# Kernel optimization log

Hardware: AMD Instinct MI355X
Metric: run time of the kernel (lower is better)

Reference implementation:

```python
import jax, jax.numpy as jnp
import numpy as np

D = 512      # d_model
P = 128      # proj_len
H = 8        # nhead
MID = 24     # middle_dim (hardcoded in module)
HD = MID // H    # head_dim = 3
HDV = D // H     # head_dim_v = 64
SCALE = HD ** -0.5   # scaling == pscaling since head_dim == phead_dim


def setup_inputs() -> dict:
    key = jax.random.key(0)
    ks = jax.random.split(key, 12)
    L, B = 2048, 16
    def w(k, o, i):
        return jax.random.normal(k, (o, i), jnp.float32) * 0.02
    def b(o):
        return jnp.zeros((o,), jnp.float32)
    return {
        "x": jax.random.normal(ks[0], (L, B, D), jnp.float32),
        "px": jax.random.normal(ks[1], (P, B, D), jnp.float32),
        "mask": jax.random.randint(ks[2], (B, L), 0, 2).astype(bool),
        "Wpq": w(ks[3], MID, D), "bpq": b(MID),
        "Wq": w(ks[4], MID, D), "bq": b(MID),
        "Wql": w(ks[5], P * H, D), "bql": b(P * H),
        "Wpk": w(ks[6], MID, D), "bpk": b(MID),
        "Wpv": w(ks[7], D, D), "bpv": b(D),
        "Wk": w(ks[8], MID, D), "bk": b(MID),
        "Wv": w(ks[9], D, D), "bv": b(D),
        "Wo": w(ks[10], D, D), "bo": b(D),
        "gamma": jnp.ones((D,), jnp.float32),
        "beta": jnp.zeros((D,), jnp.float32),
    }


def _layernorm(x, g, b, eps=1e-5):
    m = x.mean(-1, keepdims=True)
    v = ((x - m) ** 2).mean(-1, keepdims=True)
    return (x - m) / jnp.sqrt(v + eps) * g + b


def reference(x, px, mask, Wpq, bpq, Wq, bq, Wql, bql, Wpk, bpk, Wpv, bpv,
              Wk, bk, Wv, bv, Wo, bo, gamma, beta):
    L, B, _ = x.shape
    BH = B * H
    # ---- stage 1: compress length L -> P via projected attention ----
    pk = (x @ Wpk.T + bpk).reshape(L, BH, HD)     # [L, BH, hd]
    pv = (x @ Wpv.T + bpv).reshape(L, BH, HDV)    # [L, BH, hdv]
    pq = (px @ Wpq.T + bpq).reshape(P, BH, HD) * SCALE
    pqk = jnp.einsum('pnh,lnh->npl', pq, pk)      # [BH, P, L]
    pqk = pqk.reshape(B, H, P, L)
    pqk = jnp.where(mask[:, None, None, :], -jnp.inf, pqk).reshape(BH, P, L)
    pqk = jax.nn.softmax(pqk, axis=-1)            # dropout1 omitted (eval)
    pc = jnp.einsum('npl,lnv->npv', pqk, pv)      # [BH, P, hdv]
    pc = pc.transpose(1, 0, 2).reshape(P, B, D)   # compressed context
    # ---- stage 2: attention within compressed length P ----
    q_len = (x @ Wql.T + bql).reshape(L, BH, P).transpose(1, 0, 2)  # [BH, L, P]
    k = (pc @ Wk.T + bk).reshape(P, BH, HD).transpose(1, 0, 2)      # [BH, P, hd]
    v = (pc @ Wv.T + bv).reshape(P, BH, HDV).transpose(1, 0, 2)     # [BH, P, hdv]
    q = ((pc @ Wq.T + bq) * SCALE).reshape(P, BH, HD).transpose(1, 0, 2)
    aw = jax.nn.softmax(q @ k.transpose(0, 2, 1), axis=-1)  # [BH, P, P], dropout2 omitted
    attn = aw @ v                                            # [BH, P, hdv]
    attn = attn.transpose(1, 0, 2).reshape(P, B, D)
    attn = _layernorm(attn, gamma, beta)
    attn = attn.reshape(P, BH, HDV).transpose(1, 0, 2)       # [BH, P, hdv]
    # ---- stage 3: re-expand P -> L via learned length softmax ----
    ql = jax.nn.softmax(q_len, axis=-1)                      # dropout3 omitted
    out = (ql @ attn).transpose(1, 0, 2).reshape(L, B, D)
    return (out @ Wo.T + bo, pc)
```

## Files before the change

### kernel.cpp

```cpp
#include <hip/hip_runtime.h>
#include <cstdint>

#define L_    2048
#define B_    16
#define D_    512
#define P_    128
#define H_    8
#define MID_  24
#define HD_   3
#define HDV_  64
#define BH_   128
#define SCALE_ 0.57735026918962576f
#define S1C   4
#define S1L   (L_ / S1C)

typedef short  short8  __attribute__((ext_vector_type(8)));
typedef short  short4v __attribute__((ext_vector_type(4)));
typedef float  f32x4   __attribute__((ext_vector_type(4)));

__device__ __forceinline__ short f2bf(float f) {
    unsigned u = __builtin_bit_cast(unsigned, f);
    unsigned r = (u + 0x7fffu + ((u >> 16) & 1u)) >> 16;
    return (short)(unsigned short)r;
}

__device__ __forceinline__ int swz_off(int row, int chunk) {
    return row * 32 + ((chunk ^ ((row >> 1) & 3)) << 3);
}

__device__ __forceinline__ float block_reduce_sum_256(float v, volatile float* scratch) {
#pragma unroll
    for (int o = 32; o > 0; o >>= 1) v += __shfl_down(v, o, 64);
    int wid = threadIdx.x >> 6;
    if ((threadIdx.x & 63) == 0) scratch[wid] = v;
    __syncthreads();
    if (threadIdx.x == 0) scratch[4] = scratch[0] + scratch[1] + scratch[2] + scratch[3];
    __syncthreads();
    return scratch[4];
}

__global__ __launch_bounds__(256) void cvt_bf16(
    const float* __restrict__ src, short* __restrict__ dst, int n4)
{
    int i = blockIdx.x * 256 + threadIdx.x;
    if (i < n4) {
        float4 v = reinterpret_cast<const float4*>(src)[i];
        short4v o;
        o[0] = f2bf(v.x); o[1] = f2bf(v.y); o[2] = f2bf(v.z); o[3] = f2bf(v.w);
        reinterpret_cast<short4v*>(dst)[i] = o;
    }
}

__global__ __launch_bounds__(256) void gemm_bias(
    const float* __restrict__ A, const float* __restrict__ W,
    const float* __restrict__ bias, float* __restrict__ C,
    int M, int N, int K, float scale)
{
    __shared__ float As[32][36];
    __shared__ float Ws[64][36];
    const int t    = threadIdx.x;
    const int row0 = blockIdx.y * 32;
    const int col0 = blockIdx.x * 64;
    const int ty = t >> 4;
    const int tx = t & 15;
    const int lr  = t >> 3;
    const int lc4 = (t & 7) * 4;

    float acc[2][4] = {{0.f,0.f,0.f,0.f},{0.f,0.f,0.f,0.f}};

    for (int kk0 = 0; kk0 < K; kk0 += 32) {
        {
            float4 a = *reinterpret_cast<const float4*>(&A[(size_t)(row0 + lr) * K + kk0 + lc4]);
            *reinterpret_cast<float4*>(&As[lr][lc4]) = a;
        }
#pragma unroll
        for (int i = 0; i < 2; ++i) {
            int wr   = i * 32 + lr;
            int wcol = col0 + wr;
            float4 w = make_float4(0.f, 0.f, 0.f, 0.f);
            if (wcol < N)
                w = *reinterpret_cast<const float4*>(&W[(size_t)wcol * K + kk0 + lc4]);
            *reinterpret_cast<float4*>(&Ws[wr][lc4]) = w;
        }
        __syncthreads();
#pragma unroll
        for (int k4 = 0; k4 < 8; ++k4) {
            float4 a0 = *reinterpret_cast<const float4*>(&As[ty * 2][k4 * 4]);
            float4 a1 = *reinterpret_cast<const float4*>(&As[ty * 2 + 1][k4 * 4]);
#pragma unroll
            for (int ci = 0; ci < 4; ++ci) {
                float4 w = *reinterpret_cast<const float4*>(&Ws[ci * 16 + tx][k4 * 4]);
                acc[0][ci] += a0.x * w.x + a0.y * w.y + a0.z * w.z + a0.w * w.w;
                acc[1][ci] += a1.x * w.x + a1.y * w.y + a1.z * w.z + a1.w * w.w;
            }
        }
        __syncthreads();
    }
#pragma unroll
    for (int ri = 0; ri < 2; ++ri) {
        int r = row0 + ty * 2 + ri;
#pragma unroll
        for (int ci = 0; ci < 4; ++ci) {
            int c = col0 + ci * 16 + tx;
            if (c < N) C[(size_t)r * N + c] = (acc[ri][ci] + bias[c]) * scale;
        }
    }
}

__global__ __launch_bounds__(256) void gemm_bias2(
    const float* __restrict__ A,
    const float* __restrict__ W0, const float* __restrict__ b0, float* __restrict__ C0, float s0,
    const float* __restrict__ W1, const float* __restrict__ b1, float* __restrict__ C1, float s1,
    int M, int N, int K)
{
    const float* W    = blockIdx.z ? W1 : W0;
    const float* bias = blockIdx.z ? b1 : b0;
    float*       C    = blockIdx.z ? C1 : C0;
    const float scale = blockIdx.z ? s1 : s0;

    __shared__ float As[32][36];
    __shared__ float Ws[64][36];
    const int t    = threadIdx.x;
    const int row0 = blockIdx.y * 32;
    const int col0 = blockIdx.x * 64;
    const int ty = t >> 4;
    const int tx = t & 15;
    const int lr  = t >> 3;
    const int lc4 = (t & 7) * 4;

    float acc[2][4] = {{0.f,0.f,0.f,0.f},{0.f,0.f,0.f,0.f}};

    for (int kk0 = 0; kk0 < K; kk0 += 32) {
        {
            float4 a = *reinterpret_cast<const float4*>(&A[(size_t)(row0 + lr) * K + kk0 + lc4]);
            *reinterpret_cast<float4*>(&As[lr][lc4]) = a;
        }
#pragma unroll
        for (int i = 0; i < 2; ++i) {
            int wr   = i * 32 + lr;
            int wcol = col0 + wr;
            float4 w = make_float4(0.f, 0.f, 0.f, 0.f);
            if (wcol < N)
                w = *reinterpret_cast<const float4*>(&W[(size_t)wcol * K + kk0 + lc4]);
            *reinterpret_cast<float4*>(&Ws[wr][lc4]) = w;
        }
        __syncthreads();
#pragma unroll
        for (int k4 = 0; k4 < 8; ++k4) {
            float4 a0 = *reinterpret_cast<const float4*>(&As[ty * 2][k4 * 4]);
            float4 a1 = *reinterpret_cast<const float4*>(&As[ty * 2 + 1][k4 * 4]);
#pragma unroll
            for (int ci = 0; ci < 4; ++ci) {
                float4 w = *reinterpret_cast<const float4*>(&Ws[ci * 16 + tx][k4 * 4]);
                acc[0][ci] += a0.x * w.x + a0.y * w.y + a0.z * w.z + a0.w * w.w;
                acc[1][ci] += a1.x * w.x + a1.y * w.y + a1.z * w.z + a1.w * w.w;
            }
        }
        __syncthreads();
    }
#pragma unroll
    for (int ri = 0; ri < 2; ++ri) {
        int r = row0 + ty * 2 + ri;
#pragma unroll
        for (int ci = 0; ci < 4; ++ci) {
            int c = col0 + ci * 16 + tx;
            if (c < N) C[(size_t)r * N + c] = (acc[ri][ci] + bias[c]) * scale;
        }
    }
}

__global__ __launch_bounds__(256) void gemm_mfma_bt(
    const float* __restrict__ A, const short* __restrict__ Wb,
    const float* __restrict__ bias, float* __restrict__ C,
    int M, int N, int K)
{
    __shared__ __align__(16) short As[128][40];
    __shared__ __align__(16) short Bs[64][40];
    const int t    = threadIdx.x;
    const int w    = t >> 6;
    const int lane = t & 63;
    const int q    = lane >> 4;
    const int l16  = lane & 15;
    const int row0 = blockIdx.y * 128;
    const int col0 = blockIdx.x * 64;

    const int ar = t >> 1;
    const int ac = (t & 1) * 16;
    const int br = t >> 2;
    const int bc = (t & 3) * 8;

    const f32x4 z = {0.f, 0.f, 0.f, 0.f};
    f32x4 acc[2][4];
#pragma unroll
    for (int i = 0; i < 2; ++i)
#pragma unroll
        for (int j = 0; j < 4; ++j) acc[i][j] = z;

    for (int kk = 0; kk < K; kk += 32) {
        {
            const float4* ap = reinterpret_cast<const float4*>(&A[(size_t)(row0 + ar) * K + kk + ac]);
            float4 v0 = ap[0], v1 = ap[1], v2 = ap[2], v3 = ap[3];
            short8 s0, s1;
            s0[0]=f2bf(v0.x); s0[1]=f2bf(v0.y); s0[2]=f2bf(v0.z); s0[3]=f2bf(v0.w);
            s0[4]=f2bf(v1.x); s0[5]=f2bf(v1.y); s0[6]=f2bf(v1.z); s0[7]=f2bf(v1.w);
            s1[0]=f2bf(v2.x); s1[1]=f2bf(v2.y); s1[2]=f2bf(v2.z); s1[3]=f2bf(v2.w);
            s1[4]=f2bf(v3.x); s1[5]=f2bf(v3.y); s1[6]=f2bf(v3.z); s1[7]=f2bf(v3.w);
            *reinterpret_cast<short8*>(&As[ar][ac])     = s0;
            *reinterpret_cast<short8*>(&As[ar][ac + 8]) = s1;
        }
        *reinterpret_cast<short8*>(&Bs[br][bc]) =
            *reinterpret_cast<const short8*>(&Wb[(size_t)(col0 + br) * K + kk + bc]);
        __syncthreads();

        short8 af[2], bf[4];
#pragma unroll
        for (int i = 0; i < 2; ++i)
            af[i] = *reinterpret_cast<const short8*>(&As[32 * w + i * 16 + l16][q * 8]);
#pragma unroll
        for (int ct = 0; ct < 4; ++ct)
            bf[ct] = *reinterpret_cast<const short8*>(&Bs[ct * 16 + l16][q * 8]);
#pragma unroll
        for (int i = 0; i < 2; ++i)
#pragma unroll
            for (int ct = 0; ct < 4; ++ct)
                acc[i][ct] = __builtin_amdgcn_mfma_f32_16x16x32_bf16(af[i], bf[ct], acc[i][ct], 0, 0, 0);
        __syncthreads();
    }

#pragma unroll
    for (int i = 0; i < 2; ++i) {
#pragma unroll
        for (int ct = 0; ct < 4; ++ct) {
            int col = col0 + ct * 16 + l16;
            float bv = bias[col];
#pragma unroll
            for (int r = 0; r < 4; ++r) {
                int row = row0 + 32 * w + i * 16 + q * 4 + r;
                C[(size_t)row * N + col] = acc[i][ct][r] + bv;
            }
        }
    }
}

template<bool BF16OUT>
__global__ __launch_bounds__(256) void gemm_bb(
    const short* __restrict__ Ab, const short* __restrict__ Wb,
    const float* __restrict__ bias, void* __restrict__ Cout,
    int M, int N, int K)
{
    __shared__ __align__(16) short As[128 * 32];
    __shared__ __align__(16) short Bs[128 * 32];
    const int t    = threadIdx.x;
    const int w    = t >> 6;
    const int lane = t & 63;
    const int q    = lane >> 4;
    const int l16  = lane & 15;

    const int gid  = blockIdx.x;
    const int nct  = N >> 7;
    const int xcd  = gid & 7;
    const int j    = gid >> 3;
    const int row0 = (xcd + 8 * (j / nct)) * 128;
    const int col0 = (j % nct) * 128;

    const int sr  = t >> 1;
    const int sc0 = (t & 1) * 2;
    const int offS0 = swz_off(sr, sc0);
    const int offS1 = swz_off(sr, sc0 + 1);

    const f32x4 z = {0.f, 0.f, 0.f, 0.f};
    f32x4 acc[2][8];
#pragma unroll
    for (int i = 0; i < 2; ++i)
#pragma unroll
        for (int jj = 0; jj < 8; ++jj) acc[i][jj] = z;

    for (int kk = 0; kk < K; kk += 32) {
        {
            const short* ap = &Ab[(size_t)(row0 + sr) * K + kk + sc0 * 8];
            *reinterpret_cast<short8*>(&As[offS0]) = *reinterpret_cast<const short8*>(ap);
            *reinterpret_cast<short8*>(&As[offS1]) = *reinterpret_cast<const short8*>(ap + 8);
            const short* bp = &Wb[(size_t)(col0 + sr) * K + kk + sc0 * 8];
            *reinterpret_cast<short8*>(&Bs[offS0]) = *reinterpret_cast<const short8*>(bp);
            *reinterpret_cast<short8*>(&Bs[offS1]) = *reinterpret_cast<const short8*>(bp + 8);
        }
        __syncthreads();

        short8 af[2], bf[8];
#pragma unroll
        for (int i = 0; i < 2; ++i)
            af[i] = *reinterpret_cast<const short8*>(&As[swz_off(32 * w + i * 16 + l16, q)]);
#pragma unroll
        for (int ct = 0; ct < 8; ++ct)
            bf[ct] = *reinterpret_cast<const short8*>(&Bs[swz_off(ct * 16 + l16, q)]);
#pragma unroll
        for (int i = 0; i < 2; ++i)
#pragma unroll
            for (int ct = 0; ct < 8; ++ct)
                acc[i][ct] = __builtin_amdgcn_mfma_f32_16x16x32_bf16(af[i], bf[ct], acc[i][ct], 0, 0, 0);
        __syncthreads();
    }

#pragma unroll
    for (int i = 0; i < 2; ++i) {
#pragma unroll
        for (int ct = 0; ct < 8; ++ct) {
            int col = col0 + ct * 16 + l16;
            float bv = bias[col];
#pragma unroll
            for (int r = 0; r < 4; ++r) {
                int row = row0 + 32 * w + i * 16 + q * 4 + r;
                float v = acc[i][ct][r] + bv;
                if (BF16OUT)
                    ((short*)Cout)[(size_t)row * N + col] = f2bf(v);
                else
                    ((float*)Cout)[(size_t)row * N + col] = v;
            }
        }
    }
}

__global__ __launch_bounds__(512) void stage1_split(
    const float* __restrict__ pk, const float* __restrict__ pq,
    const short* __restrict__ pvb, const int* __restrict__ mask,
    float* __restrict__ pc, float* __restrict__ sumtot)
{
    __shared__ float pkt[S1L * 3];
    __shared__ float mka[S1L];
    __shared__ __align__(16) short As[P_][40];
    __shared__ __align__(16) short pvt[32][68];

    const int t = threadIdx.x;
    const int n = blockIdx.x;
    const int c = blockIdx.y;
    const int lbase = c * S1L;
    const int b = n >> 3;
    const int h = n & 7;

    {
        const int l = t;
        const float* pp = &pk[((size_t)(lbase + l) * BH_ + n) * HD_];
        pkt[l * 3 + 0] = pp[0];
        pkt[l * 3 + 1] = pp[1];
        pkt[l * 3 + 2] = pp[2];
        mka[l] = mask[b * L_ + lbase + l] ? -1e30f : 0.f;
    }

    const int p   = t >> 2;
    const int pl8 = (t & 3) * 8;
    const float pq0 = pq[((size_t)p * B_ + b) * MID_ + h * HD_ + 0];
    const float pq1 = pq[((size_t)p * B_ + b) * MID_ + h * HD_ + 1];
    const float pq2 = pq[((size_t)p * B_ + b) * MID_ + h * HD_ + 2];
    __syncthreads();

    const int lane = t & 63;
    const int w    = t >> 6;
    const int q    = lane >> 4;
    const int l16  = lane & 15;
    const int svl  = t >> 4;
    const int svc  = (t & 15) * 4;

    float psum = 0.f;
    const f32x4 z = {0.f, 0.f, 0.f, 0.f};
    f32x4 acc[4] = {z, z, z, z};

    for (int kt = 0; kt < S1L / 32; ++kt) {
        *reinterpret_cast<short4v*>(&pvt[svl][svc]) =
            *reinterpret_cast<const short4v*>(&pvb[((size_t)(lbase + kt * 32 + svl) * BH_ + n) * HDV_ + svc]);
        {
            const float* pb = &pkt[(kt * 32 + pl8) * 3];
            float kv[24], mk[8];
#pragma unroll
            for (int j = 0; j < 6; ++j)
                *reinterpret_cast<float4*>(&kv[j * 4]) = *reinterpret_cast<const float4*>(pb + j * 4);
            *reinterpret_cast<float4*>(&mk[0]) = *reinterpret_cast<const float4*>(&mka[kt * 32 + pl8]);
            *reinterpret_cast<float4*>(&mk[4]) = *reinterpret_cast<const float4*>(&mka[kt * 32 + pl8 + 4]);
            short8 a8;
#pragma unroll
            for (int j = 0; j < 8; ++j) {
                float s = pq0 * kv[j * 3] + pq1 * kv[j * 3 + 1] + pq2 * kv[j * 3 + 2] + mk[j];
                float e = __expf(s);
                psum += e;
                a8[j] = f2bf(e);
            }
            *reinterpret_cast<short8*>(&As[p][pl8]) = a8;
        }
        __syncthreads();

        short8 af = *reinterpret_cast<const short8*>(&As[w * 16 + l16][q * 8]);
#pragma unroll
        for (int ct = 0; ct < 4; ++ct) {
            short8 bf;
#pragma unroll
            for (int j = 0; j < 8; ++j) bf[j] = pvt[q * 8 + j][ct * 16 + l16];
            acc[ct] = __builtin_amdgcn_mfma_f32_16x16x32_bf16(af, bf, acc[ct], 0, 0, 0);
        }
        __syncthreads();
    }

    psum += __shfl_xor(psum, 1, 64);
    psum += __shfl_xor(psum, 2, 64);
    if ((t & 3) == 0) unsafeAtomicAdd(&sumtot[n * P_ + p], psum);

#pragma unroll
    for (int ct = 0; ct < 4; ++ct) {
        int dv = ct * 16 + l16;
#pragma unroll
        for (int r = 0; r < 4; ++r) {
            int pr = w * 16 + q * 4 + r;
            unsafeAtomicAdd(&pc[((size_t)(pr * B_ + b)) * D_ + h * HDV_ + dv], acc[ct][r]);
        }
    }
}

__global__ __launch_bounds__(256) void normalize_pc(
    float* __restrict__ pc, const float* __restrict__ sumtot)
{
    int i = blockIdx.x * 256 + threadIdx.x;
    float4 v = reinterpret_cast<float4*>(pc)[i];
    int flat = i * 4;
    int pb = flat >> 9;
    int d  = flat & 511;
    int p = pb >> 4, b = pb & 15, h = d >> 6;
    float s = 1.f / sumtot[(b * H_ + h) * P_ + p];
    v.x *= s; v.y *= s; v.z *= s; v.w *= s;
    reinterpret_cast<float4*>(pc)[i] = v;
}

__global__ __launch_bounds__(256) void stage2_attn(
    const float* __restrict__ qtmp, const float* __restrict__ ktmp,
    const float* __restrict__ vtmp, float* __restrict__ apre)
{
    __shared__ float S[32][132];
    __shared__ float ks[128][4];
    __shared__ float qs[32][4];
    __shared__ float vs[128][64];
    const int t  = threadIdx.x;
    const int n  = blockIdx.x;
    const int b  = n >> 3;
    const int h  = n & 7;
    const int p0 = blockIdx.y * 32;

    if (t < 128) {
        const float* kr = &ktmp[(size_t)(t * B_ + b) * MID_ + h * HD_];
        ks[t][0] = kr[0]; ks[t][1] = kr[1]; ks[t][2] = kr[2];
    } else if (t < 160) {
        int r = t - 128;
        const float* qr = &qtmp[(size_t)((p0 + r) * B_ + b) * MID_ + h * HD_];
        qs[r][0] = qr[0]; qs[r][1] = qr[1]; qs[r][2] = qr[2];
    }
#pragma unroll
    for (int j = 0; j < 8; ++j) {
        int idx = t + j * 256;
        int r = idx >> 4, c4 = (idx & 15) * 4;
        *reinterpret_cast<float4*>(&vs[r][c4]) =
            *reinterpret_cast<const float4*>(&vtmp[(size_t)(r * B_ + b) * D_ + h * HDV_ + c4]);
    }
    __syncthreads();

    {
        const int c  = t & 127;
        const int rg = t >> 7;
        float k0 = ks[c][0], k1 = ks[c][1], k2 = ks[c][2];
#pragma unroll
        for (int i = 0; i < 16; ++i) {
            int r = rg * 16 + i;
            S[r][c] = qs[r][0] * k0 + qs[r][1] * k1 + qs[r][2] * k2;
        }
    }
    __syncthreads();

    {
        const int srow = t >> 3;
        const int c0   = (t & 7) * 16;
        float mx = -1e30f;
#pragma unroll
        for (int i = 0; i < 16; ++i) mx = fmaxf(mx, S[srow][c0 + i]);
        mx = fmaxf(mx, __shfl_xor(mx, 1, 64));
        mx = fmaxf(mx, __shfl_xor(mx, 2, 64));
        mx = fmaxf(mx, __shfl_xor(mx, 4, 64));
        float e[16];
        float sum = 0.f;
#pragma unroll
        for (int i = 0; i < 16; ++i) { e[i] = __expf(S[srow][c0 + i] - mx); sum += e[i]; }
        sum += __shfl_xor(sum, 1, 64);
        sum += __shfl_xor(sum, 2, 64);
        sum += __shfl_xor(sum, 4, 64);
        float inv = 1.f / sum;
#pragma unroll
        for (int i = 0; i < 16; ++i) S[srow][c0 + i] = e[i] * inv;
    }
    __syncthreads();

    {
        const int dv = t & 63;
        const int pg = t >> 6;
        float acc[8] = {0.f,0.f,0.f,0.f,0.f,0.f,0.f,0.f};
        for (int pp = 0; pp < 128; pp += 4) {
            float v0 = vs[pp + 0][dv], v1 = vs[pp + 1][dv];
            float v2 = vs[pp + 2][dv], v3 = vs[pp + 3][dv];
#pragma unroll
            for (int pi = 0; pi < 8; ++pi) {
                const float4 s4 = *reinterpret_cast<const float4*>(&S[pg * 8 + pi][pp]);
                acc[pi] = fmaf(s4.x, v0, fmaf(s4.y, v1, fmaf(s4.z, v2, fmaf(s4.w, v3, acc[pi]))));
            }
        }
#pragma unroll
        for (int pi = 0; pi < 8; ++pi)
            apre[(size_t)((p0 + pg * 8 + pi) * B_ + b) * D_ + h * HDV_ + dv] = acc[pi];
    }
}

__global__ __launch_bounds__(256) void layernorm_t(
    const float* __restrict__ apre, const float* __restrict__ gamma,
    const float* __restrict__ beta, short* __restrict__ attnT2)
{
    __shared__ float red[8];
    const int t   = threadIdx.x;
    const int row = blockIdx.x;
    const int p   = row >> 4;
    const int b   = row & 15;
    float v0 = apre[(size_t)row * D_ + t];
    float v1 = apre[(size_t)row * D_ + 256 + t];
    float mean = block_reduce_sum_256(v0 + v1, red) * (1.f / D_);
    float d0 = v0 - mean, d1 = v1 - mean;
    float var  = block_reduce_sum_256(d0 * d0 + d1 * d1, red) * (1.f / D_);
    float rstd = rsqrtf(var + 1e-5f);
#pragma unroll
    for (int j = 0; j < 2; ++j) {
        int d = t + j * 256;
        int h = d >> 6, dv = d & 63;
        float v = (j ? d1 : d0) * rstd * gamma[d] + beta[d];
        attnT2[(((size_t)(b * H_ + h)) * HDV_ + dv) * P_ + p] = f2bf(v);
    }
}

__global__ __launch_bounds__(512, 4) void score_softmax(
    const short* __restrict__ xb, const short* __restrict__ Wqlb,
    const float* __restrict__ bql, short* __restrict__ probsT)
{
    __shared__ __align__(16) short As[128 * 32];
    __shared__ __align__(16) short Bs[128 * 32];
    __shared__ float reds[128][4];

    const int t    = threadIdx.x;
    const int gid  = blockIdx.x;
    const int xcd  = gid & 7;
    const int j    = gid >> 3;
    const int h    = j & 7;
    const int l0   = (xcd + 8 * (j >> 3)) * 128;

    const int lane = t & 63;
    const int w    = t >> 6;
    const int q    = lane >> 4;
    const int l16  = lane & 15;
    const int rg   = w & 3;
    const int ch   = w >> 2;
    const int sar  = t >> 2;
    const int sch  = t & 3;
    const int soff = swz_off(sar, sch);

    const f32x4 z = {0.f, 0.f, 0.f, 0.f};
    f32x4 acc[2][4];
#pragma unroll
    for (int i = 0; i < 2; ++i)
#pragma unroll
        for (int jj = 0; jj < 4; ++jj) acc[i][jj] = z;

    for (int kk = 0; kk < D_; kk += 32) {
        *reinterpret_cast<short8*>(&As[soff]) =
            *reinterpret_cast<const short8*>(&xb[(size_t)(l0 + sar) * D_ + kk + sch * 8]);
        *reinterpret_cast<short8*>(&Bs[soff]) =
            *reinterpret_cast<const short8*>(&Wqlb[(size_t)(h * P_ + sar) * D_ + kk + sch * 8]);
        __syncthreads();

        short8 af[2], bf[4];
#pragma unroll
        for (int i = 0; i < 2; ++i)
            af[i] = *reinterpret_cast<const short8*>(&Bs[swz_off(rg * 32 + i * 16 + l16, q)]);
#pragma unroll
        for (int ct = 0; ct < 4; ++ct)
            bf[ct] = *reinterpret_cast<const short8*>(&As[swz_off(ch * 64 + ct * 16 + l16, q)]);
#pragma unroll
        for (int i = 0; i < 2; ++i)
#pragma unroll
            for (int ct = 0; ct < 4; ++ct)
                acc[i][ct] = __builtin_amdgcn_mfma_f32_16x16x32_bf16(af[i], bf[ct], acc[i][ct], 0, 0, 0);
        __syncthreads();
    }

    {
        float bv[2][4];
#pragma unroll
        for (int i = 0; i < 2; ++i)
#pragma unroll
            for (int r = 0; r < 4; ++r)
                bv[i][r] = bql[h * P_ + rg * 32 + i * 16 + q * 4 + r];
#pragma unroll
        for (int i = 0; i < 2; ++i)
#pragma unroll
            for (int ct = 0; ct < 4; ++ct)
#pragma unroll
                for (int r = 0; r < 4; ++r)
                    acc[i][ct][r] += bv[i][r];
    }

    float e[4][2][4];
#pragma unroll
    for (int ct = 0; ct < 4; ++ct) {
        float s = 0.f;
#pragma unroll
        for (int i = 0; i < 2; ++i)
#pragma unroll
            for (int r = 0; r < 4; ++r) {
                float v = __expf(acc[i][ct][r]);
                e[ct][i][r] = v;
                s += v;
            }
        s += __shfl_xor(s, 16, 64);
        s += __shfl_xor(s, 32, 64);
        if (q == 0) reds[ch * 64 + ct * 16 + l16][rg] = s;
    }
    __syncthreads();

#pragma unroll
    for (int ct = 0; ct < 4; ++ct) {
        const int lc = ch * 64 + ct * 16 + l16;
        float S   = reds[lc][0] + reds[lc][1] + reds[lc][2] + reds[lc][3];
        float inv = 1.f / S;

        const int lrow = (l0 + ch * 64 + ct * 16) >> 4;
        const int b    = l16;
        short* dst = &probsT[((size_t)b * L_ + lrow) * (P_ * H_) + h * P_ + rg * 32 + q * 4];
#pragma unroll
        for (int i = 0; i < 2; ++i) {
            short4v o;
#pragma unroll
            for (int r = 0; r < 4; ++r)
                o[r] = f2bf(e[ct][i][r] * inv);
            *reinterpret_cast<short4v*>(dst + i * 16) = o;
        }
    }
}

__global__ __launch_bounds__(256) void expand_y(
    const short* __restrict__ probsT, const short* __restrict__ attnT2,
    short* __restrict__ yb)
{
    __shared__ __align__(16) short As[128 * 32];
    __shared__ __align__(16) short Bt[64][136];
    const int t    = threadIdx.x;
    const int b    = blockIdx.x >> 4;
    const int l0   = (blockIdx.x & 15) * 128;
    const int h    = blockIdx.y;
    const int lane = t & 63;
    const int w    = t >> 6;
    const int q    = lane >> 4;
    const int l16  = lane & 15;

    {
        int r = t >> 2, c = (t & 3) * 32;
        const short* src = &attnT2[(((size_t)(b * H_ + h)) * HDV_ + r) * P_ + c];
#pragma unroll
        for (int j = 0; j < 4; ++j)
            *reinterpret_cast<short8*>(&Bt[r][c + j * 8]) =
                *reinterpret_cast<const short8*>(src + j * 8);
    }

    const int ar  = t >> 1;
    const int ac0 = (t & 1) * 2;
    const int offA0 = swz_off(ar, ac0);
    const int offA1 = swz_off(ar, ac0 + 1);
    const f32x4 z = {0.f, 0.f, 0.f, 0.f};
    f32x4 acc[2][4];
#pragma unroll
    for (int i = 0; i < 2; ++i)
#pragma unroll
        for (int j = 0; j < 4; ++j) acc[i][j] = z;

    for (int ks = 0; ks < 4; ++ks) {
        const int kk = ks * 32;
        const short* ap = &probsT[((size_t)b * L_ + l0 + ar) * (P_ * H_) + h * P_ + kk + ac0 * 8];
        *reinterpret_cast<short8*>(&As[offA0]) = *reinterpret_cast<const short8*>(ap);
        *reinterpret_cast<short8*>(&As[offA1]) = *reinterpret_cast<const short8*>(ap + 8);
        __syncthreads();

        short8 af[2], bf[4];
#pragma unroll
        for (int i = 0; i < 2; ++i)
            af[i] = *reinterpret_cast<const short8*>(&As[swz_off(32 * w + i * 16 + l16, q)]);
#pragma unroll
        for (int ct = 0; ct < 4; ++ct)
            bf[ct] = *reinterpret_cast<const short8*>(&Bt[ct * 16 + l16][kk + q * 8]);
#pragma unroll
        for (int i = 0; i < 2; ++i)
#pragma unroll
            for (int ct = 0; ct < 4; ++ct)
                acc[i][ct] = __builtin_amdgcn_mfma_f32_16x16x32_bf16(af[i], bf[ct], acc[i][ct], 0, 0, 0);
        __syncthreads();
    }

#pragma unroll
    for (int i = 0; i < 2; ++i) {
#pragma unroll
        for (int ct = 0; ct < 4; ++ct) {
            int col = ct * 16 + l16;
#pragma unroll
            for (int r = 0; r < 4; ++r) {
                int row = 32 * w + i * 16 + q * 4 + r;
                yb[((size_t)(l0 + row) * B_ + b) * D_ + h * HDV_ + col] = f2bf(acc[i][ct][r]);
            }
        }
    }
}

extern "C" void kernel_launch(void* const* d_in, const int* in_sizes, int n_in,
                              void* d_out, int out_size, void* d_ws, size_t ws_size,
                              hipStream_t stream)
{
    const float* x     = (const float*)d_in[0];
    const float* px    = (const float*)d_in[1];
    const int*   mask  = (const int*)d_in[2];
    const float* Wpq   = (const float*)d_in[3];
    const float* bpq   = (const float*)d_in[4];
    const float* Wq    = (const float*)d_in[5];
    const float* bq    = (const float*)d_in[6];
    const float* Wql   = (const float*)d_in[7];
    const float* bql   = (const float*)d_in[8];
    const float* Wpk   = (const float*)d_in[9];
    const float* bpk   = (const float*)d_in[10];
    const float* Wpv   = (const float*)d_in[11];
    const float* bpv   = (const float*)d_in[12];
    const float* Wk    = (const float*)d_in[13];
    const float* bk    = (const float*)d_in[14];
    const float* Wv    = (const float*)d_in[15];
    const float* bv    = (const float*)d_in[16];
    const float* Wo    = (const float*)d_in[17];
    const float* bo    = (const float*)d_in[18];
    const float* gamma = (const float*)d_in[19];
    const float* beta  = (const float*)d_in[20];

    float* out = (float*)d_out;
    float* pc  = out + (size_t)L_ * B_ * D_;

    float* ws    = (float*)d_ws;
    float* pk    = ws;
    float* pq    = pk    + 786432;
    float* ktmp  = pq    + 49152;
    float* qtmp  = ktmp  + 49152;
    float* vtmp  = qtmp  + 49152;
    float* apre  = vtmp  + 1048576;
    short* Wpvb  = (short*)(apre + 1048576);
    short* Wob   = Wpvb + 262144;
    short* Wqlb  = Wob  + 262144;
    short* Wvb   = Wqlb + 524288;
    short* xb    = Wvb  + 262144;
    short* pvb   = xb   + 16777216;
    float* sumtot = (float*)(pvb + 16777216);
    short* yb    = xb;
    short* attnT2 = (short*)pk;
    short* probsT = (short*)d_out;

    const int MLB = L_ * B_;
    const int MPB = P_ * B_;

    cvt_bf16<<<dim3(256),   256, 0, stream>>>(Wpv, Wpvb, D_*D_/4);
    cvt_bf16<<<dim3(256),   256, 0, stream>>>(Wo,  Wob,  D_*D_/4);
    cvt_bf16<<<dim3(512),   256, 0, stream>>>(Wql, Wqlb, P_*H_*D_/4);
    cvt_bf16<<<dim3(256),   256, 0, stream>>>(Wv,  Wvb,  D_*D_/4);
    cvt_bf16<<<dim3(16384), 256, 0, stream>>>(x,   xb,   MLB*D_/4);

    hipMemsetAsync(pc, 0, (size_t)P_ * B_ * D_ * sizeof(float), stream);
    hipMemsetAsync(sumtot, 0, (size_t)BH_ * P_ * sizeof(float), stream);

    gemm_bias<<<dim3(1, MLB / 32), 256, 0, stream>>>(x,  Wpk, bpk, pk, MLB, MID_, D_, 1.f);
    gemm_bias<<<dim3(1, MPB / 32), 256, 0, stream>>>(px, Wpq, bpq, pq, MPB, MID_, D_, SCALE_);
    gemm_bb<true><<<dim3((MLB / 128) * (D_ / 128)), 256, 0, stream>>>(xb, Wpvb, bpv, pvb, MLB, D_, D_);
    stage1_split<<<dim3(BH_, S1C), 512, 0, stream>>>(pk, pq, pvb, mask, pc, sumtot);
    normalize_pc<<<dim3(P_ * B_ * D_ / 4 / 256), 256, 0, stream>>>(pc, sumtot);
    gemm_bias2<<<dim3(1, MPB / 32, 2), 256, 0, stream>>>(pc, Wk, bk, ktmp, 1.f,
                                                          Wq, bq, qtmp, SCALE_, MPB, MID_, D_);
    gemm_mfma_bt<<<dim3(D_ / 64, MPB / 128), 256, 0, stream>>>(pc, Wvb, bv, vtmp, MPB, D_, D_);
    stage2_attn<<<dim3(BH_, 4), 256, 0, stream>>>(qtmp, ktmp, vtmp, apre);
    layernorm_t<<<dim3(MPB), 256, 0, stream>>>(apre, gamma, beta, attnT2);
    score_softmax<<<dim3((MLB / 128) * H_), 512, 0, stream>>>(xb, Wqlb, bql, probsT);
    expand_y<<<dim3(B_ * 16, H_), 256, 0, stream>>>(probsT, attnT2, yb);
    gemm_bb<false><<<dim3((MLB / 128) * (D_ / 128)), 256, 0, stream>>>(yb, Wob, bo, out, MLB, D_, D_);
}
```

Measured before the change: 490.7 us.

## Fuse length-softmax scores with probability-times-attention expansion in one kernel

```diff
diff --git a/kernel.cpp b/kernel.cpp
--- a/kernel.cpp
+++ b/kernel.cpp
@@ -28,6 +28,10 @@
     return row * 32 + ((chunk ^ ((row >> 1) & 3)) << 3);
 }
 
+__device__ __forceinline__ int swzP(int row, int g) {
+    return row * 128 + ((g ^ (row & 7)) << 3);
+}
+
 __device__ __forceinline__ float block_reduce_sum_256(float v, volatile float* scratch) {
 #pragma unroll
     for (int o = 32; o > 0; o >>= 1) v += __shfl_down(v, o, 64);
@@ -535,20 +539,26 @@
     }
 }
 
-__global__ __launch_bounds__(512, 4) void score_softmax(
+__global__ __launch_bounds__(512, 4) void score_pv(
     const short* __restrict__ xb, const short* __restrict__ Wqlb,
-    const float* __restrict__ bql, short* __restrict__ probsT)
-{
-    __shared__ __align__(16) short As[128 * 32];
-    __shared__ __align__(16) short Bs[128 * 32];
+    const float* __restrict__ bql, const short* __restrict__ attnT2,
+    short* __restrict__ yf)
+{
+    __shared__ __align__(16) char smraw[128 * 128 * 2];
+    short* As = reinterpret_cast<short*>(smraw);
+    short* Bs = reinterpret_cast<short*>(smraw + 8192);
+    short* Pp = reinterpret_cast<short*>(smraw);
     __shared__ float reds[128][4];
+    __shared__ __align__(16) short Vt[64 * 128];
 
     const int t    = threadIdx.x;
     const int gid  = blockIdx.x;
     const int xcd  = gid & 7;
     const int j    = gid >> 3;
     const int h    = j & 7;
-    const int l0   = (xcd + 8 * (j >> 3)) * 128;
+    const int combo = xcd + 8 * (j >> 3);
+    const int b    = combo & 15;
+    const int l0   = (combo >> 4) * 128;
 
     const int lane = t & 63;
     const int w    = t >> 6;
@@ -560,6 +570,14 @@
     const int sch  = t & 3;
     const int soff = swz_off(sar, sch);
 
+#pragma unroll
+    for (int jj = 0; jj < 2; ++jj) {
+        int G   = t * 2 + jj;
+        int row = G >> 4, g = G & 15;
+        *reinterpret_cast<short8*>(&Vt[swzP(row, g)]) =
+            *reinterpret_cast<const short8*>(&attnT2[(((size_t)(b * H_ + h)) * HDV_ + row) * P_ + g * 8]);
+    }
+
     const f32x4 z = {0.f, 0.f, 0.f, 0.f};
     f32x4 acc[2][4];
 #pragma unroll
@@ -569,7 +587,7 @@
 
     for (int kk = 0; kk < D_; kk += 32) {
         *reinterpret_cast<short8*>(&As[soff]) =
-            *reinterpret_cast<const short8*>(&xb[(size_t)(l0 + sar) * D_ + kk + sch * 8]);
+            *reinterpret_cast<const short8*>(&xb[(size_t)((l0 + sar) * B_ + b) * D_ + kk + sch * 8]);
         *reinterpret_cast<short8*>(&Bs[soff]) =
             *reinterpret_cast<const short8*>(&Wqlb[(size_t)(h * P_ + sar) * D_ + kk + sch * 8]);
         __syncthreads();
@@ -628,87 +646,37 @@
         const int lc = ch * 64 + ct * 16 + l16;
         float S   = reds[lc][0] + reds[lc][1] + reds[lc][2] + reds[lc][3];
         float inv = 1.f / S;
-
-        const int lrow = (l0 + ch * 64 + ct * 16) >> 4;
-        const int b    = l16;
-        short* dst = &probsT[((size_t)b * L_ + lrow) * (P_ * H_) + h * P_ + rg * 32 + q * 4];
 #pragma unroll
         for (int i = 0; i < 2; ++i) {
+            int p0 = rg * 32 + i * 16 + q * 4;
             short4v o;
 #pragma unroll
             for (int r = 0; r < 4; ++r)
                 o[r] = f2bf(e[ct][i][r] * inv);
-            *reinterpret_cast<short4v*>(dst + i * 16) = o;
-        }
-    }
-}
-
-__global__ __launch_bounds__(256) void expand_y(
-    const short* __restrict__ probsT, const short* __restrict__ attnT2,
-    short* __restrict__ yb)
-{
-    __shared__ __align__(16) short As[128 * 32];
-    __shared__ __align__(16) short Bt[64][136];
-    const int t    = threadIdx.x;
-    const int b    = blockIdx.x >> 4;
-    const int l0   = (blockIdx.x & 15) * 128;
-    const int h    = blockIdx.y;
-    const int lane = t & 63;
-    const int w    = t >> 6;
-    const int q    = lane >> 4;
-    const int l16  = lane & 15;
+            *reinterpret_cast<short4v*>(&Pp[swzP(lc, p0 >> 3) + (p0 & 7)]) = o;
+        }
+    }
+    __syncthreads();
 
     {
-        int r = t >> 2, c = (t & 3) * 32;
-        const short* src = &attnT2[(((size_t)(b * H_ + h)) * HDV_ + r) * P_ + c];
-#pragma unroll
-        for (int j = 0; j < 4; ++j)
-            *reinterpret_cast<short8*>(&Bt[r][c + j * 8]) =
-                *reinterpret_cast<const short8*>(src + j * 8);
-    }
-
-    const int ar  = t >> 1;
-    const int ac0 = (t & 1) * 2;
-    const int offA0 = swz_off(ar, ac0);
-    const int offA1 = swz_off(ar, ac0 + 1);
-    const f32x4 z = {0.f, 0.f, 0.f, 0.f};
-    f32x4 acc[2][4];
-#pragma unroll
-    for (int i = 0; i < 2; ++i)
-#pragma unroll
-        for (int j = 0; j < 4; ++j) acc[i][j] = z;
-
-    for (int ks = 0; ks < 4; ++ks) {
-        const int kk = ks * 32;
-        const short* ap = &probsT[((size_t)b * L_ + l0 + ar) * (P_ * H_) + h * P_ + kk + ac0 * 8];
-        *reinterpret_cast<short8*>(&As[offA0]) = *reinterpret_cast<const short8*>(ap);
-        *reinterpret_cast<short8*>(&As[offA1]) = *reinterpret_cast<const short8*>(ap + 8);
-        __syncthreads();
-
-        short8 af[2], bf[4];
-#pragma unroll
-        for (int i = 0; i < 2; ++i)
-            af[i] = *reinterpret_cast<const short8*>(&As[swz_off(32 * w + i * 16 + l16, q)]);
-#pragma unroll
-        for (int ct = 0; ct < 4; ++ct)
-            bf[ct] = *reinterpret_cast<const short8*>(&Bt[ct * 16 + l16][kk + q * 8]);
-#pragma unroll
-        for (int i = 0; i < 2; ++i)
-#pragma unroll
-            for (int ct = 0; ct < 4; ++ct)
-                acc[i][ct] = __builtin_amdgcn_mfma_f32_16x16x32_bf16(af[i], bf[ct], acc[i][ct], 0, 0, 0);
-        __syncthreads();
-    }
-
-#pragma unroll
-    for (int i = 0; i < 2; ++i) {
+        f32x4 acc2[4] = {z, z, z, z};
+        const int arow = 16 * w + l16;
+#pragma unroll
+        for (int ks = 0; ks < 4; ++ks) {
+            short8 pa = *reinterpret_cast<const short8*>(&Pp[swzP(arow, ks * 4 + q)]);
+#pragma unroll
+            for (int ct = 0; ct < 4; ++ct) {
+                short8 vb = *reinterpret_cast<const short8*>(&Vt[swzP(ct * 16 + l16, ks * 4 + q)]);
+                acc2[ct] = __builtin_amdgcn_mfma_f32_16x16x32_bf16(pa, vb, acc2[ct], 0, 0, 0);
+            }
+        }
 #pragma unroll
         for (int ct = 0; ct < 4; ++ct) {
-            int col = ct * 16 + l16;
+            int dv = ct * 16 + l16;
 #pragma unroll
             for (int r = 0; r < 4; ++r) {
-                int row = 32 * w + i * 16 + q * 4 + r;
-                yb[((size_t)(l0 + row) * B_ + b) * D_ + h * HDV_ + col] = f2bf(acc[i][ct][r]);
+                int lrow = 16 * w + q * 4 + r;
+                yf[(size_t)((l0 + lrow) * B_ + b) * D_ + h * HDV_ + dv] = f2bf(acc2[ct][r]);
             }
         }
     }
@@ -757,9 +725,8 @@
     short* xb    = Wvb  + 262144;
     short* pvb   = xb   + 16777216;
     float* sumtot = (float*)(pvb + 16777216);
-    short* yb    = xb;
+    short* yf    = pvb;
     short* attnT2 = (short*)pk;
-    short* probsT = (short*)d_out;
 
     const int MLB = L_ * B_;
     const int MPB = P_ * B_;
@@ -783,7 +750,6 @@
     gemm_mfma_bt<<<dim3(D_ / 64, MPB / 128), 256, 0, stream>>>(pc, Wvb, bv, vtmp, MPB, D_, D_);
     stage2_attn<<<dim3(BH_, 4), 256, 0, stream>>>(qtmp, ktmp, vtmp, apre);
     layernorm_t<<<dim3(MPB), 256, 0, stream>>>(apre, gamma, beta, attnT2);
-    score_softmax<<<dim3((MLB / 128) * H_), 512, 0, stream>>>(xb, Wqlb, bql, probsT);
-    expand_y<<<dim3(B_ * 16, H_), 256, 0, stream>>>(probsT, attnT2, yb);
-    gemm_bb<false><<<dim3((MLB / 128) * (D_ / 128)), 256, 0, stream>>>(yb, Wob, bo, out, MLB, D_, D_);
-}
+    score_pv<<<dim3((MLB / 128) * H_), 512, 0, stream>>>(xb, Wqlb, bql, attnT2, yf);
+    gemm_bb<false><<<dim3((MLB / 128) * (D_ / 128)), 256, 0, stream>>>(yf, Wob, bo, out, MLB, D_, D_);
+}
```

New measurement: 467.9 us. 4.6% less time.
